# Performance work log

Measured on AMD Instinct MI355X. Metric: run time of the kernel, lower is better.

The kernel has to match this reference:

```python
import jax, jax.numpy as jnp
import numpy as np

EPS = 1e-07
ORTH_LAMBDA = 0.1
KAMA = 1.0


def setup_inputs() -> dict:
    key = jax.random.key(0)
    ks = jax.random.split(key, 10)
    b, c, h, w, n = 8, 128, 128, 128, 16
    s = 0.05  # weight init scale
    return {
        "x":     jax.random.normal(ks[0], (b, c, h, w), jnp.float32),
        "Wsa":   jax.random.normal(ks[1], (c, c), jnp.float32) * s,
        "bsa":   jnp.zeros((c,), jnp.float32),
        "Wr":    jax.random.normal(ks[2], (c, c), jnp.float32) * s,
        "br":    jnp.zeros((c,), jnp.float32),
        "kn":    jax.random.normal(ks[3], (n, c), jnp.float32),  # (nClass, in_c, 1, 1) squeezed
        "Wo":    jax.random.normal(ks[4], (c, c), jnp.float32) * s,
        "bo":    jnp.zeros((c,), jnp.float32),
        "alpha": jnp.ones((1, n, 1), jnp.float32) * 0.1,
        "sigma": jnp.ones((1,), jnp.float32) * 0.5,  # torch inits 0; nonzero so out != x
    }


def reference(x, Wsa, bsa, Wr, br, kn, Wo, bo, alpha, sigma):
    b, c, h, w = x.shape
    n = kn.shape[0]
    hw = h * w

    conv1x1 = lambda W, bb: jnp.einsum('oc,bchw->bohw', W, x) + bb[:, None, None]
    xsa = conv1x1(Wsa, bsa)                       # (b,c,h,w)
    xr = conv1x1(Wr, br)                          # (b,c,h,w)
    xo = conv1x1(Wo, bo)                          # (b,c,h,w)
    xn = jnp.einsum('nc,bchw->bnhw', kn, x)       # (b,n,h,w), no bias

    # ---- orthogonality loss over class kernels ----
    sym = kn @ kn.T                               # (n,n)
    nrm = jnp.sqrt(jnp.sum(kn ** 2, axis=-1, keepdims=True))  # (n,1)
    loss = sym / (nrm @ nrm.T + EPS) - jnp.eye(n, dtype=x.dtype)
    orth_loss = ORTH_LAMBDA * jnp.log(jnp.sum(loss ** 2) + 1.0)

    xsa_r = xsa.reshape(b, c, hw)
    xr_r = xr.reshape(b, c, hw)
    xn_r = xn.reshape(b, n, hw)

    # ---- cosine-normalized class-channel relation ----
    relation = jnp.einsum('bnk,bck->bnc', xn_r, xr_r)            # (b,n,c)
    norm_xr = jnp.sqrt(jnp.sum(xr_r ** 2, axis=-1, keepdims=True))  # (b,c,1)
    norm_xn = jnp.sqrt(jnp.sum(xn_r ** 2, axis=-1, keepdims=True))  # (b,n,1)
    relation_norm = relation / (norm_xn @ jnp.swapaxes(norm_xr, 1, 2) + EPS)

    # ---- channel self-attention regularizer ----
    rela = jnp.einsum('bik,bjk->bij', xsa_r, xsa_r)              # (b,c,c)
    factor = rela * (1.0 - jnp.eye(c, dtype=x.dtype))
    regular = jax.nn.softmax(jnp.mean(factor, axis=1, keepdims=True), axis=-1)  # (b,1,c)

    alpha_c = jnp.clip(alpha, 0.0, 1.0)                          # (1,n,1)
    relation_norm = (relation_norm + alpha_c * regular) / KAMA
    att = jax.nn.softmax(relation_norm, axis=1)                  # (b,n,c)

    # ---- fused attention-weighted group norm (no (b,n,c,h,w) materialization)
    # hot_area[b,n,c,h,w] = xo[b,c,h,w] * att[b,n,c]; reductions over (c,h,w)
    s1 = jnp.sum(xo, axis=(2, 3))                                # (b,c) sum_hw xo
    s2 = jnp.sum(xo ** 2, axis=(2, 3))                           # (b,c) sum_hw xo^2
    cnt = jnp.sum(att, axis=2) * hw + EPS                        # (b,n)
    hot_sum = jnp.einsum('bnc,bc->bn', att, s1)                  # (b,n)
    fo_mean = hot_sum / cnt                                      # (b,n)
    sq = jnp.einsum('bnc,bc->bn', att ** 2, s2) - 2.0 * fo_mean * hot_sum \
         + (fo_mean ** 2) * (c * hw)
    fo_std = jnp.sqrt(sq / cnt)                                  # (b,n)

    # out[b,c,h,w] = sum_n (xo - mean)/(std+eps) * att = xo*A - B
    inv = 1.0 / (fo_std + EPS)                                   # (b,n)
    A = jnp.einsum('bnc,bn->bc', att, inv)                       # (b,c)
    B = jnp.einsum('bnc,bn->bc', att, fo_mean * inv)             # (b,c)
    out = x + sigma * (xo * A[:, :, None, None] - B[:, :, None, None])
    return out, orth_loss
```

## Files before the change

kernel.cpp:

```cpp
#include <hip/hip_runtime.h>
#include <hip/hip_bf16.h>

#define B_   8
#define C_   128
#define HW_  16384
#define N_   16
#define EPS_ 1e-7f

typedef unsigned short u16;
typedef __attribute__((ext_vector_type(8))) short s8v;
typedef __attribute__((ext_vector_type(4))) short s4v;
typedef __attribute__((ext_vector_type(4))) float f4v;

__device__ __forceinline__ u16 f2b(float f) {
  union { __hip_bfloat16 b; u16 u; } cv; cv.b = __float2bfloat16(f); return cv.u;
}
__device__ __forceinline__ float b2f(u16 u) {
  union { float f; unsigned int i; } cv; cv.i = ((unsigned int)u) << 16; return cv.f;
}
__device__ __forceinline__ float wredsum(float v) {
#pragma unroll
  for (int o = 32; o > 0; o >>= 1) v += __shfl_xor(v, o, 64);
  return v;
}
__device__ __forceinline__ float wredmax(float v) {
#pragma unroll
  for (int o = 32; o > 0; o >>= 1) v = fmaxf(v, __shfl_xor(v, o, 64));
  return v;
}

#define XSB 512
__global__ __launch_bounds__(512, 4) void k_gram(
    const float* __restrict__ x, float* __restrict__ pbuf, float* __restrict__ psx,
    const float* __restrict__ Wsa, const float* __restrict__ kn,
    const float* __restrict__ Wo, float* __restrict__ u,
    float* __restrict__ loss_out, u16* __restrict__ wo_bf) {
  __shared__ u16 Xb[C_ * 256];
  const int tid = threadIdx.x;
  const int b = blockIdx.y;

  if (blockIdx.x == 64) {
    if (b == 0) {
      if (tid < C_) {
        float s = 0.f;
        for (int i = 0; i < C_; ++i) s += Wsa[i * C_ + tid];
        u[tid] = s;
      }
    } else if (b == 1) {
      float* smf = (float*)Xb;
      const int i = tid >> 4, j = tid & 15;
      float s = 0.f;
      if (tid < 256) {
        for (int c = 0; c < C_; ++c) s += kn[i * C_ + c] * kn[j * C_ + c];
        if (i == j) smf[i] = sqrtf(s);
      }
      __syncthreads();
      float l2 = 0.f;
      if (tid < 256) {
        float l = s / (smf[i] * smf[j] + EPS_) - (i == j ? 1.f : 0.f);
        l2 = l * l;
      }
      float wv = wredsum(l2);
      if ((tid & 63) == 0) smf[16 + (tid >> 6)] = wv;
      __syncthreads();
      if (tid == 0) {
        float t = 0.f;
        for (int k = 0; k < 8; ++k) t += smf[16 + k];
        loss_out[0] = 0.1f * logf(t + 1.f);
      }
    } else if (b == 2) {
#pragma unroll
      for (int j = 0; j < 8; ++j) {
        int f = tid + 512 * j;
        float4 v = ((const float4*)Wo)[f];
        s4v s; s[0] = (short)f2b(v.x); s[1] = (short)f2b(v.y);
        s[2] = (short)f2b(v.z); s[3] = (short)f2b(v.w);
        ((s4v*)wo_bf)[f] = s;
      }
    }
    return;
  }

  const int p0 = blockIdx.x * 256;
  const int lane = tid & 63;
  const int w = tid >> 6;
  const int m = lane & 15, q = lane >> 4;
  const int rb = (w & 3) * 32, cb = (w >> 2) * 64;

  const float* xb = x + (size_t)b * C_ * HW_;
  const int l32 = tid & 31;
  const int rbase = tid >> 5;
  const float* ro = xb + (size_t)rbase * HW_ + p0 + 4 * l32;
  char* lds = (char*)Xb;

  float4 v[8], v2[8];
#pragma unroll
  for (int j = 0; j < 8; ++j) v[j]  = *(const float4*)(ro + (size_t)(16 * j) * HW_);
#pragma unroll
  for (int j = 0; j < 8; ++j) v2[j] = *(const float4*)(ro + (size_t)(16 * j) * HW_ + 128);

  const int swc = (rbase & 7) << 4;
  float rs[8];
#pragma unroll
  for (int j = 0; j < 8; ++j) {
    const int c = rbase + 16 * j;
    s4v s; s[0] = (short)f2b(v[j].x); s[1] = (short)f2b(v[j].y);
    s[2] = (short)f2b(v[j].z); s[3] = (short)f2b(v[j].w);
    *(s4v*)(lds + c * XSB + ((8 * l32) ^ swc)) = s;
    rs[j] = v[j].x + v[j].y + v[j].z + v[j].w;
  }
#pragma unroll
  for (int j = 0; j < 8; ++j) {
    const int c = rbase + 16 * j;
    s4v s; s[0] = (short)f2b(v2[j].x); s[1] = (short)f2b(v2[j].y);
    s[2] = (short)f2b(v2[j].z); s[3] = (short)f2b(v2[j].w);
    *(s4v*)(lds + c * XSB + ((256 + 8 * l32) ^ swc)) = s;
    rs[j] += v2[j].x + v2[j].y + v2[j].z + v2[j].w;
  }
#pragma unroll
  for (int o = 16; o > 0; o >>= 1)
#pragma unroll
    for (int j = 0; j < 8; ++j) rs[j] += __shfl_xor(rs[j], o, 64);
  if (l32 == 0) {
#pragma unroll
    for (int j = 0; j < 8; ++j)
      psx[(blockIdx.x * B_ + b) * C_ + rbase + 16 * j] = rs[j];
  }
  __syncthreads();

  f4v acc[2][4];
#pragma unroll
  for (int a = 0; a < 2; ++a)
#pragma unroll
    for (int c2 = 0; c2 < 4; ++c2) acc[a][c2] = (f4v){0.f, 0.f, 0.f, 0.f};

  const int swf = (m & 7) << 4;
#pragma unroll
  for (int s = 0; s < 8; ++s) {
    const int off = (64 * s + 16 * q) ^ swf;
    s8v Af[2], Bf[4];
#pragma unroll
    for (int a = 0; a < 2; ++a)
      Af[a] = *(const s8v*)(lds + (rb + 16 * a + m) * XSB + off);
#pragma unroll
    for (int c2 = 0; c2 < 4; ++c2)
      Bf[c2] = *(const s8v*)(lds + (cb + 16 * c2 + m) * XSB + off);
#pragma unroll
    for (int a = 0; a < 2; ++a)
#pragma unroll
      for (int c2 = 0; c2 < 4; ++c2)
        acc[a][c2] = __builtin_amdgcn_mfma_f32_16x16x32_bf16(Af[a], Bf[c2], acc[a][c2], 0, 0, 0);
  }

  float* pg = pbuf + ((size_t)(blockIdx.x * B_ + b) << 14);
#pragma unroll
  for (int a = 0; a < 2; ++a)
#pragma unroll
    for (int c2 = 0; c2 < 4; ++c2)
#pragma unroll
      for (int r = 0; r < 4; ++r) {
        int row = rb + 16 * a + 4 * q + r;
        int col = cb + 16 * c2 + m;
        pg[row * C_ + col] = acc[a][c2][r];
      }
}

__global__ __launch_bounds__(128) void k_greduce(const float4* __restrict__ pbuf4,
                                                 const float* __restrict__ psx,
                                                 float4* __restrict__ G4,
                                                 float* __restrict__ sx) {
  const int blk = blockIdx.x;
  if (blk < 256) {
    const int gid = blk * 128 + threadIdx.x;
    const int b = gid >> 12, idx4 = gid & 4095;
    float4 s = {0.f, 0.f, 0.f, 0.f};
#pragma unroll 16
    for (int ch = 0; ch < 64; ++ch) {
      float4 p = pbuf4[((size_t)(ch * B_ + b) << 12) + idx4];
      s.x += p.x; s.y += p.y; s.z += p.z; s.w += p.w;
    }
    G4[gid] = s;
  } else {
    const int tt = (blk - 256) * 128 + threadIdx.x;
    const int b = tt >> 7, c = tt & 127;
    float s = 0.f;
#pragma unroll 16
    for (int ch = 0; ch < 64; ++ch) s += psx[(ch * B_ + b) * C_ + c];
    sx[tt] = s;
  }
}

__global__ __launch_bounds__(64) void k_cols(
    const float* __restrict__ G, const float* __restrict__ sx,
    const float* __restrict__ Wr, const float* __restrict__ Wsa,
    const float* __restrict__ Wo, const float* __restrict__ kn,
    const float* __restrict__ u,
    float* diagR, float* diagSA, float* colsumSA, float* diagO,
    float* prv, float* psav, float* pov, float* rel, float* diagN, float* ksx) {
  const int b = blockIdx.y;
  const int col = blockIdx.x;
  const int lane = threadIdx.x;
  const float* Gb = G + b * C_ * C_;
  const float4* g0 = (const float4*)(Gb + lane * C_);
  const float4* g1 = (const float4*)(Gb + (64 + lane) * C_);
  const float sx0 = sx[b * C_ + lane], sx1 = sx[b * C_ + 64 + lane];

  if (col < C_) {
    const float4* wr = (const float4*)(Wr + col * C_);
    const float4* wa = (const float4*)(Wsa + col * C_);
    const float4* wo = (const float4*)(Wo + col * C_);
    float t0r = 0, t1r = 0, t0a = 0, t1a = 0, t0o = 0, t1o = 0;
    for (int c = 0; c < 32; ++c) {
      float4 a0 = g0[c], a1 = g1[c];
      float4 vr = wr[c], va = wa[c], vo = wo[c];
      t0r += a0.x * vr.x + a0.y * vr.y + a0.z * vr.z + a0.w * vr.w;
      t1r += a1.x * vr.x + a1.y * vr.y + a1.z * vr.z + a1.w * vr.w;
      t0a += a0.x * va.x + a0.y * va.y + a0.z * va.z + a0.w * va.w;
      t1a += a1.x * va.x + a1.y * va.y + a1.z * va.z + a1.w * va.w;
      t0o += a0.x * vo.x + a0.y * vo.y + a0.z * vo.z + a0.w * vo.w;
      t1o += a1.x * vo.x + a1.y * vo.y + a1.z * vo.z + a1.w * vo.w;
    }
    float wr0 = Wr[col * C_ + lane], wr1 = Wr[col * C_ + 64 + lane];
    float wa0 = Wsa[col * C_ + lane], wa1 = Wsa[col * C_ + 64 + lane];
    float wo0 = Wo[col * C_ + lane], wo1 = Wo[col * C_ + 64 + lane];
    float u0 = u[lane], u1 = u[64 + lane];
    float dR = wredsum(wr0 * t0r + wr1 * t1r);
    float pR = wredsum(wr0 * sx0 + wr1 * sx1);
    float dA = wredsum(wa0 * t0a + wa1 * t1a);
    float cA = wredsum(u0 * t0a + u1 * t1a);
    float pA = wredsum(wa0 * sx0 + wa1 * sx1);
    float dO = wredsum(wo0 * t0o + wo1 * t1o);
    float pO = wredsum(wo0 * sx0 + wo1 * sx1);
    float rl[N_];
#pragma unroll
    for (int n = 0; n < N_; ++n)
      rl[n] = wredsum(kn[n * C_ + lane] * t0r + kn[n * C_ + 64 + lane] * t1r);
    if (lane == 0) {
      diagR[b * C_ + col] = dR;  prv[b * C_ + col] = pR;
      diagSA[b * C_ + col] = dA; colsumSA[b * C_ + col] = cA; psav[b * C_ + col] = pA;
      diagO[b * C_ + col] = dO;  pov[b * C_ + col] = pO;
      for (int n = 0; n < N_; ++n) rel[(b * N_ + n) * C_ + col] = rl[n];
    }
  } else {
    const int n = col - C_;
    const float4* wk = (const float4*)(kn + n * C_);
    float t0 = 0, t1 = 0;
    for (int c = 0; c < 32; ++c) {
      float4 a0 = g0[c], a1 = g1[c], vk = wk[c];
      t0 += a0.x * vk.x + a0.y * vk.y + a0.z * vk.z + a0.w * vk.w;
      t1 += a1.x * vk.x + a1.y * vk.y + a1.z * vk.z + a1.w * vk.w;
    }
    float k0v = kn[n * C_ + lane], k1v = kn[n * C_ + 64 + lane];
    float dN = wredsum(k0v * t0 + k1v * t1);
    float kx = wredsum(k0v * sx0 + k1v * sx1);
    if (lane == 0) { diagN[b * N_ + n] = dN; ksx[b * N_ + n] = kx; }
  }
}

__global__ __launch_bounds__(128) void k_asm(
    const float* diagR, const float* diagSA, const float* colsumSA, const float* diagO,
    const float* prv, const float* psav, const float* pov,
    const float* rel, const float* diagN, const float* ksx,
    const float* br, const float* bo, const float* bsa, const float* alpha,
    float* Aout, float* Bout) {
  const int b = blockIdx.x;
  const int t = threadIdx.x;
  __shared__ float rb2[2];
  __shared__ float att_s[C_][N_ + 1];
  __shared__ float s1_s[C_], s2_s[C_];
  __shared__ float inv_s[N_], fmi_s[N_];
  const float hw = (float)HW_;
  const float bsa_c = bsa[t], br_c = br[t], bo_c = bo[t];
  const float psa_c = psav[b * C_ + t], pr_c = prv[b * C_ + t], po_c = pov[b * C_ + t];

  float bsum, psum, mx, ssum;
  { float wv = wredsum(bsa_c); if ((t & 63) == 0) rb2[t >> 6] = wv; __syncthreads();
    bsum = rb2[0] + rb2[1]; __syncthreads(); }
  { float wv = wredsum(psa_c); if ((t & 63) == 0) rb2[t >> 6] = wv; __syncthreads();
    psum = rb2[0] + rb2[1]; __syncthreads(); }

  const float nxr = sqrtf(fmaxf(diagR[b * C_ + t] + 2.f * br_c * pr_c + hw * br_c * br_c, 0.f));
  s1_s[t] = po_c + hw * bo_c;
  s2_s[t] = diagO[b * C_ + t] + 2.f * bo_c * po_c + hw * bo_c * bo_c;
  const float colsum = colsumSA[b * C_ + t] + bsum * psa_c + bsa_c * (psum + hw * bsum);
  const float diagv = diagSA[b * C_ + t] + 2.f * bsa_c * psa_c + hw * bsa_c * bsa_c;
  const float fm = (colsum - diagv) * (1.f / (float)C_);

  { float wv = wredmax(fm); if ((t & 63) == 0) rb2[t >> 6] = wv; __syncthreads();
    mx = fmaxf(rb2[0], rb2[1]); __syncthreads(); }
  const float ee = expf(fm - mx);
  { float wv = wredsum(ee); if ((t & 63) == 0) rb2[t >> 6] = wv; __syncthreads();
    ssum = rb2[0] + rb2[1]; __syncthreads(); }
  const float reg = ee / ssum;

  float r[N_];
  float rmax = -1e30f;
#pragma unroll
  for (int n = 0; n < N_; ++n) {
    float al = fminf(fmaxf(alpha[n], 0.f), 1.f);
    float nxn = sqrtf(fmaxf(diagN[b * N_ + n], 0.f));
    float rv = (rel[(b * N_ + n) * C_ + t] + br_c * ksx[b * N_ + n]) / (nxn * nxr + EPS_) + al * reg;
    r[n] = rv; rmax = fmaxf(rmax, rv);
  }
  float es = 0.f;
#pragma unroll
  for (int n = 0; n < N_; ++n) { r[n] = expf(r[n] - rmax); es += r[n]; }
  const float ies = 1.f / es;
#pragma unroll
  for (int n = 0; n < N_; ++n) att_s[t][n] = r[n] * ies;
  __syncthreads();

  {
    const int nn = t >> 3, g = t & 7;
    float sa = 0.f, sh = 0.f, sq = 0.f;
#pragma unroll 4
    for (int c = g; c < C_; c += 8) {
      float a = att_s[c][nn];
      sa += a; sh += a * s1_s[c]; sq += a * a * s2_s[c];
    }
#pragma unroll
    for (int o = 4; o > 0; o >>= 1) {
      sa += __shfl_xor(sa, o, 64);
      sh += __shfl_xor(sh, o, 64);
      sq += __shfl_xor(sq, o, 64);
    }
    if (g == 0) {
      float cnt = sa * hw + EPS_;
      float fmean = sh / cnt;
      float sqv = sq - 2.f * fmean * sh + fmean * fmean * ((float)C_ * hw);
      float fstd = sqrtf(fmaxf(sqv, 0.f) / cnt);
      float inv = 1.f / (fstd + EPS_);
      inv_s[nn] = inv; fmi_s[nn] = fmean * inv;
    }
  }
  __syncthreads();

  float Ac = 0.f, Bc = 0.f;
#pragma unroll
  for (int n = 0; n < N_; ++n) { float a = att_s[t][n]; Ac += a * inv_s[n]; Bc += a * fmi_s[n]; }
  Aout[b * C_ + t] = Ac; Bout[b * C_ + t] = Bc;
}

__global__ __launch_bounds__(512, 4) void k_out(
    const float* __restrict__ x, const u16* __restrict__ wo_bf,
    const float* __restrict__ bo, const float* __restrict__ Aws,
    const float* __restrict__ Bws, const float* __restrict__ sig,
    float* __restrict__ out) {
  const int b = blockIdx.y;
  __shared__ u16 Xt[128 * 128];
  __shared__ float As[C_], Bs[C_], bos[C_];
  const int tid = threadIdx.x, lane = tid & 63, w = tid >> 6;
  const int n = lane & 15, q = lane >> 4;

  if (tid < C_) { As[tid] = Aws[b * C_ + tid]; Bs[tid] = Bws[b * C_ + tid]; bos[tid] = bo[tid]; }
  const float sg = sig[0];

  s8v af[4];
#pragma unroll
  for (int s = 0; s < 4; ++s)
    af[s] = *(const s8v*)(wo_bf + (16 * w + n) * C_ + 32 * s + 8 * q);

  const float* xb = x + (size_t)b * C_ * HW_;
  float* ob = out + (size_t)b * C_ * HW_;
  const int pqd = tid & 31;
  const int co  = tid >> 5;
  const int p0 = blockIdx.x * 256;
  char* lds = (char*)Xt;

  float4 v[8];
  const float* src0 = xb + (size_t)(8 * co) * HW_ + p0 + 4 * pqd;
#pragma unroll
  for (int r = 0; r < 8; ++r) v[r] = *(const float4*)(src0 + (size_t)r * HW_);

#pragma unroll 1
  for (int pt = 0; pt < 2; ++pt) {
    const int p = p0 + 128 * pt;
    {
      const float* vf = (const float*)v;
#pragma unroll
      for (int pp = 0; pp < 4; ++pp) {
        const int row = 4 * pqd + pp;
        s8v s;
#pragma unroll
        for (int r = 0; r < 8; ++r) s[r] = (short)f2b(vf[4 * r + pp]);
        *(s8v*)(lds + row * 256 + ((16 * co) ^ ((row & 7) << 4))) = s;
      }
    }
    __syncthreads();
    if (pt == 0) {
      const float* src1 = src0 + 128;
#pragma unroll
      for (int r = 0; r < 8; ++r) v[r] = *(const float4*)(src1 + (size_t)r * HW_);
    }

    f4v acc[8];
#pragma unroll
    for (int p2 = 0; p2 < 8; ++p2) acc[p2] = (f4v){0.f, 0.f, 0.f, 0.f};
#pragma unroll
    for (int s = 0; s < 4; ++s) {
      const int off = 64 * s + 16 * q;
#pragma unroll
      for (int p2 = 0; p2 < 8; ++p2) {
        const int row = 16 * p2 + n;
        s8v bfr = *(const s8v*)(lds + row * 256 + (off ^ ((row & 7) << 4)));
        acc[p2] = __builtin_amdgcn_mfma_f32_16x16x32_bf16(af[s], bfr, acc[p2], 0, 0, 0);
      }
    }

#pragma unroll
    for (int p2 = 0; p2 < 8; ++p2)
#pragma unroll
      for (int r = 0; r < 4; ++r) {
        int o = 16 * w + 4 * q + r;
        size_t idx = (size_t)o * HW_ + p + 16 * p2 + n;
        float xo = acc[p2][r] + bos[o];
        ob[idx] = xb[idx] + sg * (xo * As[o] - Bs[o]);
      }
    if (pt == 0) __syncthreads();
  }
}

extern "C" void kernel_launch(void* const* d_in, const int* in_sizes, int n_in,
                              void* d_out, int out_size, void* d_ws, size_t ws_size,
                              hipStream_t stream) {
  (void)in_sizes; (void)n_in; (void)out_size; (void)ws_size;
  const float* x     = (const float*)d_in[0];
  const float* Wsa   = (const float*)d_in[1];
  const float* bsa   = (const float*)d_in[2];
  const float* Wr    = (const float*)d_in[3];
  const float* br    = (const float*)d_in[4];
  const float* kn    = (const float*)d_in[5];
  const float* Wo    = (const float*)d_in[6];
  const float* bo    = (const float*)d_in[7];
  const float* alpha = (const float*)d_in[8];
  const float* sigma = (const float*)d_in[9];
  float* out = (float*)d_out;
  float* ws  = (float*)d_ws;

  float* G        = ws;
  float* sx       = ws + 131072;
  float* diagR    = ws + 132096;
  float* diagSA   = ws + 133120;
  float* colsumSA = ws + 134144;
  float* diagO    = ws + 135168;
  float* prv      = ws + 136192;
  float* psav     = ws + 137216;
  float* pov      = ws + 138240;
  float* rel      = ws + 139264;
  float* diagN    = ws + 155648;
  float* ksx      = ws + 155776;
  float* u        = ws + 155904;
  float* Aw       = ws + 156032;
  float* Bw       = ws + 157056;
  u16*   wo_bf    = (u16*)(ws + 158080);

  float* pbuf = out;
  float* psx  = out + 8388608;

  k_gram<<<dim3(65, 8), 512, 0, stream>>>(x, pbuf, psx, Wsa, kn, Wo, u,
      out + (size_t)B_ * C_ * HW_, wo_bf);
  k_greduce<<<264, 128, 0, stream>>>((const float4*)pbuf, psx, (float4*)G, sx);
  k_cols<<<dim3(144, 8), 64, 0, stream>>>(G, sx, Wr, Wsa, Wo, kn, u,
      diagR, diagSA, colsumSA, diagO, prv, psav, pov, rel, diagN, ksx);
  k_asm<<<8, 128, 0, stream>>>(diagR, diagSA, colsumSA, diagO, prv, psav, pov,
      rel, diagN, ksx, br, bo, bsa, alpha, Aw, Bw);
  k_out<<<dim3(64, 8), 512, 0, stream>>>(x, wo_bf, bo, Aw, Bw, sigma, out);
}
```

Before: 210.6 us.

## Restructure gram and output kernels for coalesced stores and smaller LDS tiles

k_gram now stages x in two 128-pixel halves in a padded LDS tile instead of one 256-pixel swizzled tile. Each half is loaded and the MFMA gram is accumulated in turn. Per-channel sums are now taken from the bf16 LDS copy rather than the fp32 registers, which changes sx precision slightly. k_out processes 128 pixels per block on a doubled grid and transposes the MFMA results through LDS so the output is written with coalesced float4 stores reusing the register copy of x instead of reloading it. It also folds sigma, A, B and bias into two per-channel coefficients computed in k_asm.

```diff
diff --git a/kernel.cpp b/kernel.cpp
--- a/kernel.cpp
+++ b/kernel.cpp
@@ -29,13 +29,13 @@
   return v;
 }
 
-#define XSB 512
+#define XS_ 132
 __global__ __launch_bounds__(512, 4) void k_gram(
     const float* __restrict__ x, float* __restrict__ pbuf, float* __restrict__ psx,
     const float* __restrict__ Wsa, const float* __restrict__ kn,
     const float* __restrict__ Wo, float* __restrict__ u,
     float* __restrict__ loss_out, u16* __restrict__ wo_bf) {
-  __shared__ u16 Xb[C_ * 256];
+  __shared__ u16 Xb[C_ * XS_];
   const int tid = threadIdx.x;
   const int b = blockIdx.y;
 
@@ -87,69 +87,59 @@
   const int m = lane & 15, q = lane >> 4;
   const int rb = (w & 3) * 32, cb = (w >> 2) * 64;
 
+  f4v acc[2][4];
+#pragma unroll
+  for (int a = 0; a < 2; ++a)
+#pragma unroll
+    for (int c2 = 0; c2 < 4; ++c2) acc[a][c2] = (f4v){0.f, 0.f, 0.f, 0.f};
+
+  float sxp = 0.f;
   const float* xb = x + (size_t)b * C_ * HW_;
-  const int l32 = tid & 31;
-  const int rbase = tid >> 5;
-  const float* ro = xb + (size_t)rbase * HW_ + p0 + 4 * l32;
-  char* lds = (char*)Xb;
-
-  float4 v[8], v2[8];
-#pragma unroll
-  for (int j = 0; j < 8; ++j) v[j]  = *(const float4*)(ro + (size_t)(16 * j) * HW_);
-#pragma unroll
-  for (int j = 0; j < 8; ++j) v2[j] = *(const float4*)(ro + (size_t)(16 * j) * HW_ + 128);
-
-  const int swc = (rbase & 7) << 4;
-  float rs[8];
-#pragma unroll
-  for (int j = 0; j < 8; ++j) {
-    const int c = rbase + 16 * j;
-    s4v s; s[0] = (short)f2b(v[j].x); s[1] = (short)f2b(v[j].y);
-    s[2] = (short)f2b(v[j].z); s[3] = (short)f2b(v[j].w);
-    *(s4v*)(lds + c * XSB + ((8 * l32) ^ swc)) = s;
-    rs[j] = v[j].x + v[j].y + v[j].z + v[j].w;
-  }
-#pragma unroll
-  for (int j = 0; j < 8; ++j) {
-    const int c = rbase + 16 * j;
-    s4v s; s[0] = (short)f2b(v2[j].x); s[1] = (short)f2b(v2[j].y);
-    s[2] = (short)f2b(v2[j].z); s[3] = (short)f2b(v2[j].w);
-    *(s4v*)(lds + c * XSB + ((256 + 8 * l32) ^ swc)) = s;
-    rs[j] += v2[j].x + v2[j].y + v2[j].z + v2[j].w;
-  }
-#pragma unroll
-  for (int o = 16; o > 0; o >>= 1)
-#pragma unroll
-    for (int j = 0; j < 8; ++j) rs[j] += __shfl_xor(rs[j], o, 64);
-  if (l32 == 0) {
-#pragma unroll
-    for (int j = 0; j < 8; ++j)
-      psx[(blockIdx.x * B_ + b) * C_ + rbase + 16 * j] = rs[j];
-  }
-  __syncthreads();
-
-  f4v acc[2][4];
-#pragma unroll
-  for (int a = 0; a < 2; ++a)
-#pragma unroll
-    for (int c2 = 0; c2 < 4; ++c2) acc[a][c2] = (f4v){0.f, 0.f, 0.f, 0.f};
-
-  const int swf = (m & 7) << 4;
-#pragma unroll
-  for (int s = 0; s < 8; ++s) {
-    const int off = (64 * s + 16 * q) ^ swf;
-    s8v Af[2], Bf[4];
-#pragma unroll
-    for (int a = 0; a < 2; ++a)
-      Af[a] = *(const s8v*)(lds + (rb + 16 * a + m) * XSB + off);
-#pragma unroll
-    for (int c2 = 0; c2 < 4; ++c2)
-      Bf[c2] = *(const s8v*)(lds + (cb + 16 * c2 + m) * XSB + off);
-#pragma unroll
-    for (int a = 0; a < 2; ++a)
+  const float* ro = xb + (size_t)(tid >> 5) * HW_ + p0 + 4 * (tid & 31);
+
+  float4 v[8];
+#pragma unroll
+  for (int j = 0; j < 8; ++j) v[j] = *(const float4*)(ro + (size_t)(16 * j) * HW_);
+
+#pragma unroll
+  for (int t = 0; t < 2; ++t) {
+#pragma unroll
+    for (int j = 0; j < 8; ++j) {
+      int c = (tid >> 5) + 16 * j;
+      s4v s; s[0] = (short)f2b(v[j].x); s[1] = (short)f2b(v[j].y);
+      s[2] = (short)f2b(v[j].z); s[3] = (short)f2b(v[j].w);
+      *(s4v*)(&Xb[c * XS_ + 4 * (tid & 31)]) = s;
+    }
+    __syncthreads();
+    if (t == 0) {
+#pragma unroll
+      for (int j = 0; j < 8; ++j) v[j] = *(const float4*)(ro + (size_t)(16 * j) * HW_ + 128);
+    }
+    if (tid < C_) {
+#pragma unroll
+      for (int kk = 0; kk < 16; ++kk) {
+        s8v vv = *(const s8v*)(&Xb[tid * XS_ + 8 * kk]);
+#pragma unroll
+        for (int e = 0; e < 8; ++e) sxp += b2f((u16)vv[e]);
+      }
+    }
+#pragma unroll
+    for (int s = 0; s < 4; ++s) {
+      const int k0 = 32 * s;
+      s8v Af[2], Bf[4];
+#pragma unroll
+      for (int a = 0; a < 2; ++a)
+        Af[a] = *(const s8v*)(&Xb[(rb + 16 * a + m) * XS_ + k0 + 8 * q]);
 #pragma unroll
       for (int c2 = 0; c2 < 4; ++c2)
-        acc[a][c2] = __builtin_amdgcn_mfma_f32_16x16x32_bf16(Af[a], Bf[c2], acc[a][c2], 0, 0, 0);
+        Bf[c2] = *(const s8v*)(&Xb[(cb + 16 * c2 + m) * XS_ + k0 + 8 * q]);
+#pragma unroll
+      for (int a = 0; a < 2; ++a)
+#pragma unroll
+        for (int c2 = 0; c2 < 4; ++c2)
+          acc[a][c2] = __builtin_amdgcn_mfma_f32_16x16x32_bf16(Af[a], Bf[c2], acc[a][c2], 0, 0, 0);
+    }
+    __syncthreads();
   }
 
   float* pg = pbuf + ((size_t)(blockIdx.x * B_ + b) << 14);
@@ -163,6 +153,7 @@
         int col = cb + 16 * c2 + m;
         pg[row * C_ + col] = acc[a][c2][r];
       }
+  if (tid < C_) psx[(blockIdx.x * B_ + b) * C_ + tid] = sxp;
 }
 
 __global__ __launch_bounds__(128) void k_greduce(const float4* __restrict__ pbuf4,
@@ -262,7 +253,7 @@
     const float* prv, const float* psav, const float* pov,
     const float* rel, const float* diagN, const float* ksx,
     const float* br, const float* bo, const float* bsa, const float* alpha,
-    float* Aout, float* Bout) {
+    const float* sigma, float* C1out, float* C0out) {
   const int b = blockIdx.x;
   const int t = threadIdx.x;
   __shared__ float rb2[2];
@@ -338,85 +329,105 @@
   float Ac = 0.f, Bc = 0.f;
 #pragma unroll
   for (int n = 0; n < N_; ++n) { float a = att_s[t][n]; Ac += a * inv_s[n]; Bc += a * fmi_s[n]; }
-  Aout[b * C_ + t] = Ac; Bout[b * C_ + t] = Bc;
+  const float sg = sigma[0];
+  C1out[b * C_ + t] = sg * Ac;
+  C0out[b * C_ + t] = sg * (Ac * bo_c - Bc);
 }
 
 __global__ __launch_bounds__(512, 4) void k_out(
     const float* __restrict__ x, const u16* __restrict__ wo_bf,
-    const float* __restrict__ bo, const float* __restrict__ Aws,
-    const float* __restrict__ Bws, const float* __restrict__ sig,
+    const float* __restrict__ c1g, const float* __restrict__ c0g,
     float* __restrict__ out) {
+  __shared__ f4v smem4[4096];
+  char* lds = (char*)smem4;
   const int b = blockIdx.y;
-  __shared__ u16 Xt[128 * 128];
-  __shared__ float As[C_], Bs[C_], bos[C_];
   const int tid = threadIdx.x, lane = tid & 63, w = tid >> 6;
   const int n = lane & 15, q = lane >> 4;
-
-  if (tid < C_) { As[tid] = Aws[b * C_ + tid]; Bs[tid] = Bws[b * C_ + tid]; bos[tid] = bo[tid]; }
-  const float sg = sig[0];
+  const int co = tid >> 5;
+  const int l  = tid & 31;
+  const int p0 = blockIdx.x * 128;
 
   s8v af[4];
 #pragma unroll
   for (int s = 0; s < 4; ++s)
     af[s] = *(const s8v*)(wo_bf + (16 * w + n) * C_ + 32 * s + 8 * q);
 
+  float c1[8], c0[8];
+#pragma unroll
+  for (int r = 0; r < 8; ++r) {
+    c1[r] = c1g[b * C_ + 8 * co + r];
+    c0[r] = c0g[b * C_ + 8 * co + r];
+  }
+
   const float* xb = x + (size_t)b * C_ * HW_;
   float* ob = out + (size_t)b * C_ * HW_;
-  const int pqd = tid & 31;
-  const int co  = tid >> 5;
-  const int p0 = blockIdx.x * 256;
-  char* lds = (char*)Xt;
 
   float4 v[8];
-  const float* src0 = xb + (size_t)(8 * co) * HW_ + p0 + 4 * pqd;
-#pragma unroll
-  for (int r = 0; r < 8; ++r) v[r] = *(const float4*)(src0 + (size_t)r * HW_);
-
-#pragma unroll 1
-  for (int pt = 0; pt < 2; ++pt) {
-    const int p = p0 + 128 * pt;
-    {
-      const float* vf = (const float*)v;
-#pragma unroll
-      for (int pp = 0; pp < 4; ++pp) {
-        const int row = 4 * pqd + pp;
-        s8v s;
-#pragma unroll
-        for (int r = 0; r < 8; ++r) s[r] = (short)f2b(vf[4 * r + pp]);
-        *(s8v*)(lds + row * 256 + ((16 * co) ^ ((row & 7) << 4))) = s;
-      }
-    }
-    __syncthreads();
-    if (pt == 0) {
-      const float* src1 = src0 + 128;
-#pragma unroll
-      for (int r = 0; r < 8; ++r) v[r] = *(const float4*)(src1 + (size_t)r * HW_);
-    }
-
-    f4v acc[8];
-#pragma unroll
-    for (int p2 = 0; p2 < 8; ++p2) acc[p2] = (f4v){0.f, 0.f, 0.f, 0.f};
-#pragma unroll
-    for (int s = 0; s < 4; ++s) {
-      const int off = 64 * s + 16 * q;
-#pragma unroll
-      for (int p2 = 0; p2 < 8; ++p2) {
-        const int row = 16 * p2 + n;
-        s8v bfr = *(const s8v*)(lds + row * 256 + (off ^ ((row & 7) << 4)));
-        acc[p2] = __builtin_amdgcn_mfma_f32_16x16x32_bf16(af[s], bfr, acc[p2], 0, 0, 0);
-      }
-    }
-
-#pragma unroll
-    for (int p2 = 0; p2 < 8; ++p2)
-#pragma unroll
-      for (int r = 0; r < 4; ++r) {
-        int o = 16 * w + 4 * q + r;
-        size_t idx = (size_t)o * HW_ + p + 16 * p2 + n;
-        float xo = acc[p2][r] + bos[o];
-        ob[idx] = xb[idx] + sg * (xo * As[o] - Bs[o]);
-      }
-    if (pt == 0) __syncthreads();
+  const float* src = xb + (size_t)(8 * co) * HW_ + p0 + 4 * l;
+#pragma unroll
+  for (int r = 0; r < 8; ++r) v[r] = *(const float4*)(src + (size_t)r * HW_);
+
+  {
+    const float* vf = (const float*)v;
+#pragma unroll
+    for (int pp = 0; pp < 4; ++pp) {
+      const int row = 4 * l + pp;
+      s8v s;
+#pragma unroll
+      for (int r = 0; r < 8; ++r) s[r] = (short)f2b(vf[4 * r + pp]);
+      *(s8v*)(lds + row * 256 + ((16 * co) ^ (((row ^ (row >> 2)) & 7) << 4))) = s;
+    }
+  }
+  __syncthreads();
+
+  f4v acc[8];
+#pragma unroll
+  for (int p2 = 0; p2 < 8; ++p2) acc[p2] = (f4v){0.f, 0.f, 0.f, 0.f};
+#pragma unroll
+  for (int s = 0; s < 4; ++s) {
+#pragma unroll
+    for (int p2 = 0; p2 < 8; ++p2) {
+      const int row = 16 * p2 + n;
+      s8v bfr = *(const s8v*)(lds + row * 256 +
+                              ((64 * s + 16 * q) ^ (((row ^ (row >> 2)) & 7) << 4)));
+      acc[p2] = __builtin_amdgcn_mfma_f32_16x16x32_bf16(af[s], bfr, acc[p2], 0, 0, 0);
+    }
+  }
+  __syncthreads();
+
+#pragma unroll
+  for (int p2 = 0; p2 < 8; ++p2) {
+    const int px = 16 * p2 + n;
+    *(f4v*)(lds + px * 512 + ((64 * w + 16 * q) ^ (((px ^ (px >> 2)) & 7) << 4))) = acc[p2];
+  }
+  __syncthreads();
+
+  f4v ra[4], rb_[4];
+#pragma unroll
+  for (int pp = 0; pp < 4; ++pp) {
+    const int px = 4 * l + pp;
+    const int g = ((px ^ (px >> 2)) & 7) << 4;
+    ra[pp]  = *(const f4v*)(lds + px * 512 + ((32 * co) ^ g));
+    rb_[pp] = *(const f4v*)(lds + px * 512 + ((32 * co + 16) ^ g));
+  }
+  float* obp = ob + (size_t)(8 * co) * HW_ + p0 + 4 * l;
+#pragma unroll
+  for (int r = 0; r < 4; ++r) {
+    float4 o4;
+    o4.x = v[r].x + c1[r] * ra[0][r] + c0[r];
+    o4.y = v[r].y + c1[r] * ra[1][r] + c0[r];
+    o4.z = v[r].z + c1[r] * ra[2][r] + c0[r];
+    o4.w = v[r].w + c1[r] * ra[3][r] + c0[r];
+    *(float4*)(obp + (size_t)r * HW_) = o4;
+  }
+#pragma unroll
+  for (int r = 0; r < 4; ++r) {
+    float4 o4;
+    o4.x = v[4 + r].x + c1[4 + r] * rb_[0][r] + c0[4 + r];
+    o4.y = v[4 + r].y + c1[4 + r] * rb_[1][r] + c0[4 + r];
+    o4.z = v[4 + r].z + c1[4 + r] * rb_[2][r] + c0[4 + r];
+    o4.w = v[4 + r].w + c1[4 + r] * rb_[3][r] + c0[4 + r];
+    *(float4*)(obp + (size_t)(4 + r) * HW_) = o4;
   }
 }
 
@@ -450,8 +461,8 @@
   float* diagN    = ws + 155648;
   float* ksx      = ws + 155776;
   float* u        = ws + 155904;
-  float* Aw       = ws + 156032;
-  float* Bw       = ws + 157056;
+  float* C1w      = ws + 156032;
+  float* C0w      = ws + 157056;
   u16*   wo_bf    = (u16*)(ws + 158080);
 
   float* pbuf = out;
@@ -463,6 +474,6 @@
   k_cols<<<dim3(144, 8), 64, 0, stream>>>(G, sx, Wr, Wsa, Wo, kn, u,
       diagR, diagSA, colsumSA, diagO, prv, psav, pov, rel, diagN, ksx);
   k_asm<<<8, 128, 0, stream>>>(diagR, diagSA, colsumSA, diagO, prv, psav, pov,
-      rel, diagN, ksx, br, bo, bsa, alpha, Aw, Bw);
-  k_out<<<dim3(64, 8), 512, 0, stream>>>(x, wo_bf, bo, Aw, Bw, sigma, out);
-}
+      rel, diagN, ksx, br, bo, bsa, alpha, sigma, C1w, C0w);
+  k_out<<<dim3(128, 8), 512, 0, stream>>>(x, wo_bf, C1w, C0w, out);
+}
```

Measured after the change: 188.4 us. 10.5% less time.
